# Kernel optimization log

Hardware: AMD Instinct MI355X
Metric: run time of the kernel (lower is better)

Reference implementation:

```python
import jax, jax.numpy as jnp
import numpy as np

LN_EPS = 1e-5

def setup_inputs() -> dict:
    key = jax.random.key(0)
    ks = jax.random.split(key, 7)
    B, S, D = 16, 2048, 512
    scale_g = 1.0 / np.sqrt(2 * D)
    scale_c = 1.0 / np.sqrt(2 * D)
    return {
        "points": jax.random.normal(ks[0], (B, S, D), dtype=jnp.float32),
        "W_gate": jax.random.uniform(ks[1], (2 * D, 2 * D), jnp.float32, -scale_g, scale_g),
        "b_gate": jax.random.uniform(ks[2], (2 * D,), jnp.float32, -scale_g, scale_g),
        "W_cand": jax.random.uniform(ks[3], (2 * D, D), jnp.float32, -scale_c, scale_c),
        "b_cand": jax.random.uniform(ks[4], (D,), jnp.float32, -scale_c, scale_c),
        "gamma": jnp.ones((D,), jnp.float32),
        "beta": jnp.zeros((D,), jnp.float32),
    }

def _layer_norm(x, gamma, beta):
    mu = jnp.mean(x, axis=-1, keepdims=True)
    var = jnp.mean(jnp.square(x - mu), axis=-1, keepdims=True)
    return (x - mu) * jax.lax.rsqrt(var + LN_EPS) * gamma + beta

def reference(points, W_gate, b_gate, W_cand, b_cand, gamma, beta):
    B, S, D = points.shape
    h0 = jnp.zeros((B, D), dtype=points.dtype)

    def step(h, p_t):  # p_t: [B, D]
        combined = jnp.concatenate([p_t, h], axis=1)          # [B, 2D]
        gates = combined @ W_gate + b_gate                    # [B, 2D]
        r = jax.nn.sigmoid(gates[:, :D])
        z = jax.nn.sigmoid(gates[:, D:])
        cand_in = jnp.concatenate([p_t, r * h], axis=1)       # [B, 2D]
        c = jnp.tanh(cand_in @ W_cand + b_cand)               # [B, D]
        h_new = (1.0 - z) * h + z * c
        return h_new, h_new

    _, states = jax.lax.scan(step, h0, jnp.swapaxes(points, 0, 1))  # [S, B, D]
    states = jnp.swapaxes(states, 0, 1)                             # [B, S, D]
    displacement = states - points
    deformed = points + displacement
    return _layer_norm(deformed, gamma, beta)
```

## Files before the change

kernel.cpp:

```cpp
#include <hip/hip_runtime.h>


typedef _Float16 half8 __attribute__((ext_vector_type(8)));
typedef _Float16 half4 __attribute__((ext_vector_type(4)));
typedef float floatx4 __attribute__((ext_vector_type(4)));
typedef int int4v __attribute__((ext_vector_type(4)));

#define NBLK 16
#define TPB 256
#define S_LEN 2048

#define SZ_WPK (96ull * 16 * 64 * 8 * 2)
#define OFF_WHPK 0ull
#define OFF_WXPK (OFF_WHPK + SZ_WPK)
#define OFF_HBUF (OFF_WXPK + SZ_WPK)
#define OFF_CNT (OFF_HBUF + 16384ull)
#define OFF_RH (OFF_CNT + 16384ull)
#define OFF_XGT (OFF_RH + 16384ull)

__device__ __forceinline__ float sigmoid_f(float x) {
  return 1.f / (1.f + __expf(-x));
}
__device__ __forceinline__ float tanh_f(float x) {
  x = fminf(15.f, fmaxf(-15.f, x));
  float e = __expf(2.f * x);
  return (e - 1.f) / (e + 1.f);
}

__device__ __forceinline__ void ld4_cg(const _Float16* p, int4v (&f)[4]) {
  asm volatile(
      "global_load_dwordx4 %0, %4, off sc0 sc1\n\t"
      "global_load_dwordx4 %1, %4, off offset:64 sc0 sc1\n\t"
      "global_load_dwordx4 %2, %4, off offset:128 sc0 sc1\n\t"
      "global_load_dwordx4 %3, %4, off offset:192 sc0 sc1\n\t"
      "s_waitcnt vmcnt(0)"
      : "=&v"(f[0]), "=&v"(f[1]), "=&v"(f[2]), "=&v"(f[3])
      : "v"(p)
      : "memory");
}
__device__ __forceinline__ void st_cg_u16(_Float16* p, _Float16 v) {
  unsigned u = (unsigned)__builtin_bit_cast(unsigned short, v);
  asm volatile("global_store_short %0, %1, off sc0 sc1" ::"v"(p), "v"(u)
               : "memory");
}
__device__ __forceinline__ void vwait() {
  asm volatile("s_waitcnt vmcnt(0)" ::: "memory");
}
__device__ __forceinline__ void st_flag(unsigned* p, unsigned v) {
  asm volatile("global_store_dword %0, %1, off sc0 sc1" ::"v"(p), "v"(v)
               : "memory");
}
__device__ __forceinline__ unsigned ld_flag(const unsigned* p) {
  unsigned v;
  asm volatile("global_load_dword %0, %1, off sc0 sc1\n\t"
               "s_waitcnt vmcnt(0)"
               : "=v"(v)
               : "v"(p)
               : "memory");
  return v;
}

__device__ __forceinline__ void gbar(unsigned* __restrict__ flags, int j,
                                     unsigned token, int wave, int lane) {
  __syncthreads();
  if (wave == 0) {
    if (lane == 0) st_flag(flags + j, token);
    const unsigned* fp = flags + (lane & 15);
    for (;;) {
      unsigned v = ld_flag(fp);
      if (__all((int)(v >= token))) break;
    }
  }
  __syncthreads();
}

__global__ void pack_kernel(const float* __restrict__ Wg,
                            const float* __restrict__ Wc,
                            _Float16* __restrict__ Whpk,
                            _Float16* __restrict__ Wxpk) {
  int unit = blockIdx.x * 4 + (threadIdx.x >> 6);
  int lane = threadIdx.x & 63;
  int set = (unit >= 1536) ? 1 : 0;
  int rem = unit - set * 1536;
  int tile = rem >> 4, kc = rem & 15;
  int kb = kc * 32 + ((lane >> 4) << 3);
  int n = lane & 15;
  int row0 = set ? 0 : 512;
  half8 w;
  if (tile < 64) {
    int col = tile * 16 + n;
#pragma unroll
    for (int jj = 0; jj < 8; ++jj)
      w[jj] = (_Float16)Wg[(size_t)(row0 + kb + jj) * 1024 + col];
  } else {
    int col = (tile - 64) * 16 + n;
#pragma unroll
    for (int jj = 0; jj < 8; ++jj)
      w[jj] = (_Float16)Wc[(size_t)(row0 + kb + jj) * 512 + col];
  }
  _Float16* dst = set ? Wxpk : Whpk;
  *(half8*)(dst + ((size_t)rem * 64 + lane) * 8) = w;
}

__global__ __launch_bounds__(TPB) void xgemm_kernel(
    const float* __restrict__ points, const float* __restrict__ b_gate,
    const float* __restrict__ b_cand, const _Float16* __restrict__ Wxpk,
    _Float16* __restrict__ xgt) {
  __shared__ _Float16 x_lds[16][520];
  const int tid = threadIdx.x;
  const int wave = tid >> 6, lane = tid & 63;
  const int ln15 = lane & 15, q = lane >> 4;
  const int t = blockIdx.x;
  const int m = tid & 15, ch = tid >> 4;

  const float* xp = points + ((size_t)m * S_LEN + t) * 512 + ch * 32;
#pragma unroll
  for (int u = 0; u < 4; ++u) {
    float4 f0 = ((const float4*)xp)[2 * u];
    float4 f1 = ((const float4*)xp)[2 * u + 1];
    half8 hv;
    hv[0] = (_Float16)f0.x; hv[1] = (_Float16)f0.y;
    hv[2] = (_Float16)f0.z; hv[3] = (_Float16)f0.w;
    hv[4] = (_Float16)f1.x; hv[5] = (_Float16)f1.y;
    hv[6] = (_Float16)f1.z; hv[7] = (_Float16)f1.w;
    *(half8*)&x_lds[m][ch * 32 + u * 8] = hv;
  }
  __syncthreads();

  for (int tile = wave; tile < 96; tile += 4) {
    const _Float16* W = Wxpk + (size_t)tile * 8192;
    floatx4 a0 = {0.f, 0.f, 0.f, 0.f}, a1 = {0.f, 0.f, 0.f, 0.f};
#pragma unroll
    for (int kc = 0; kc < 16; kc += 2) {
      a0 = __builtin_amdgcn_mfma_f32_16x16x32_f16(
          *(const half8*)&x_lds[ln15][kc * 32 + q * 8],
          *(const half8*)(W + ((size_t)kc * 64 + lane) * 8), a0, 0, 0, 0);
      a1 = __builtin_amdgcn_mfma_f32_16x16x32_f16(
          *(const half8*)&x_lds[ln15][(kc + 1) * 32 + q * 8],
          *(const half8*)(W + ((size_t)(kc + 1) * 64 + lane) * 8), a1, 0, 0, 0);
    }
    float bias = (tile < 64) ? b_gate[tile * 16 + ln15]
                             : b_cand[(tile - 64) * 16 + ln15];
    half4 o;
#pragma unroll
    for (int i = 0; i < 4; ++i) o[i] = (_Float16)(a0[i] + a1[i] + bias);
    *(half4*)(xgt + (((size_t)t * 96 + tile) * 16 + ln15) * 16 + q * 4) = o;
  }
}

__global__ __launch_bounds__(TPB, 1) void rec_kernel(
    const _Float16* __restrict__ Whpk, const _Float16* __restrict__ xgt,
    _Float16* __restrict__ h_buf, _Float16* __restrict__ rh_buf,
    unsigned* __restrict__ flags, float* __restrict__ out) {
  __shared__ int4v hsh[1024];
  __shared__ float z_lds[16][36];

  const int tid = threadIdx.x;
  const int wave = tid >> 6, lane = tid & 63;
  const int ln15 = lane & 15, q = lane >> 4;
  const int j = blockIdx.x;

  const int twA = (wave < 2) ? (2 * j + wave) : (32 + 2 * j + (wave - 2));
  const int twB = 64 + 2 * j + (wave & 1);
  const int colA = 32 * j + 16 * (wave & 1) + ln15;

  half8 wA[16], wB[16];
  {
    const _Float16* sA = Whpk + (size_t)twA * 8192 + lane * 8;
#pragma unroll
    for (int kc = 0; kc < 16; ++kc) wA[kc] = *(const half8*)(sA + kc * 512);
  }
  if (wave < 2) {
    const _Float16* sB = Whpk + (size_t)twB * 8192 + lane * 8;
#pragma unroll
    for (int kc = 0; kc < 16; ++kc) wB[kc] = *(const half8*)(sB + kc * 512);
  }

  const _Float16* h_stage = h_buf + ln15 * 512 + q * 8 + wave * 128;
  const _Float16* rh_stage = rh_buf + ln15 * 512 + q * 8 + wave * 128;
  _Float16* rh_st = rh_buf + (q * 4) * 512 + colA;
  _Float16* h_st = h_buf + (q * 4) * 512 + colA;

  const _Float16* xga_p = xgt + ((size_t)twA * 16 + ln15) * 16 + q * 4;
  const _Float16* xcb_p = xgt + ((size_t)twB * 16 + ln15) * 16 + q * 4;
  half4 xga = *(const half4*)xga_p;
  half4 xcb = {0, 0, 0, 0};
  if (wave < 2) xcb = *(const half4*)xcb_p;

  float hreg[4] = {0.f, 0.f, 0.f, 0.f};

  for (int t = 0; t < S_LEN; ++t) {
    const size_t pn = (size_t)((t + 1 < S_LEN) ? t + 1 : t) * 24576;

    {
      int4v f[4];
      ld4_cg(h_stage, f);
#pragma unroll
      for (int u = 0; u < 4; ++u) hsh[(4 * wave + u) * 64 + lane] = f[u];
    }
    __syncthreads();

    floatx4 a0 = {0.f, 0.f, 0.f, 0.f}, a1 = {0.f, 0.f, 0.f, 0.f};
#pragma unroll
    for (int kc = 0; kc < 16; kc += 2) {
      a0 = __builtin_amdgcn_mfma_f32_16x16x32_f16(
          __builtin_bit_cast(half8, hsh[kc * 64 + lane]), wA[kc], a0, 0, 0, 0);
      a1 = __builtin_amdgcn_mfma_f32_16x16x32_f16(
          __builtin_bit_cast(half8, hsh[(kc + 1) * 64 + lane]), wA[kc + 1], a1,
          0, 0, 0);
    }
    if (wave < 2) {
#pragma unroll
      for (int i = 0; i < 4; ++i) {
        float r = sigmoid_f(a0[i] + a1[i] + (float)xga[i]);
        st_cg_u16(rh_st + i * 512, (_Float16)(r * hreg[i]));
      }
      vwait();
    } else {
#pragma unroll
      for (int i = 0; i < 4; ++i)
        z_lds[q * 4 + i][16 * (wave - 2) + ln15] =
            sigmoid_f(a0[i] + a1[i] + (float)xga[i]);
    }
    gbar(flags, j, 2u * t + 1u, wave, lane);

    {
      int4v f[4];
      ld4_cg(rh_stage, f);
#pragma unroll
      for (int u = 0; u < 4; ++u) hsh[(4 * wave + u) * 64 + lane] = f[u];
    }
    __syncthreads();

    if (wave < 2) {
      floatx4 b0 = {0.f, 0.f, 0.f, 0.f}, b1 = {0.f, 0.f, 0.f, 0.f};
#pragma unroll
      for (int kc = 0; kc < 16; kc += 2) {
        b0 = __builtin_amdgcn_mfma_f32_16x16x32_f16(
            __builtin_bit_cast(half8, hsh[kc * 64 + lane]), wB[kc], b0, 0, 0,
            0);
        b1 = __builtin_amdgcn_mfma_f32_16x16x32_f16(
            __builtin_bit_cast(half8, hsh[(kc + 1) * 64 + lane]), wB[kc + 1],
            b1, 0, 0, 0);
      }
      float hn_s[4];
#pragma unroll
      for (int i = 0; i < 4; ++i) {
        float cv = tanh_f(b0[i] + b1[i] + (float)xcb[i]);
        float zz = z_lds[q * 4 + i][16 * wave + ln15];
        float hn = hreg[i] + zz * (cv - hreg[i]);
        _Float16 hh = (_Float16)hn;
        hreg[i] = (float)hh;
        st_cg_u16(h_st + i * 512, hh);
        hn_s[i] = hn;
      }
      vwait();
      xga = *(const half4*)(xga_p + pn);
      xcb = *(const half4*)(xcb_p + pn);
#pragma unroll
      for (int i = 0; i < 4; ++i)
        out[((size_t)(q * 4 + i) * S_LEN + t) * 512 + colA] = hn_s[i];
    } else {
      xga = *(const half4*)(xga_p + pn);
    }
    gbar(flags, j, 2u * t + 2u, wave, lane);
  }
}

__global__ void ln_kernel(float* __restrict__ out, const float* __restrict__ gamma,
                          const float* __restrict__ beta) {
  int gw = (blockIdx.x * blockDim.x + threadIdx.x) >> 6;
  int lane = threadIdx.x & 63;
  int nw = (gridDim.x * blockDim.x) >> 6;
  float4 ga = ((const float4*)(gamma + lane * 8))[0];
  float4 gb = ((const float4*)(gamma + lane * 8))[1];
  float4 ba = ((const float4*)(beta + lane * 8))[0];
  float4 bb = ((const float4*)(beta + lane * 8))[1];
  for (int r = gw; r < 16 * S_LEN; r += nw) {
    float* p = out + (size_t)r * 512 + lane * 8;
    float4 v0 = ((float4*)p)[0], v1 = ((float4*)p)[1];
    float s = v0.x + v0.y + v0.z + v0.w + v1.x + v1.y + v1.z + v1.w;
    float sq = v0.x * v0.x + v0.y * v0.y + v0.z * v0.z + v0.w * v0.w +
               v1.x * v1.x + v1.y * v1.y + v1.z * v1.z + v1.w * v1.w;
#pragma unroll
    for (int off = 32; off > 0; off >>= 1) {
      s += __shfl_xor(s, off);
      sq += __shfl_xor(sq, off);
    }
    float mean = s * (1.f / 512.f);
    float var = sq * (1.f / 512.f) - mean * mean;
    float rstd = rsqrtf(var + 1e-5f);
    v0.x = (v0.x - mean) * rstd * ga.x + ba.x;
    v0.y = (v0.y - mean) * rstd * ga.y + ba.y;
    v0.z = (v0.z - mean) * rstd * ga.z + ba.z;
    v0.w = (v0.w - mean) * rstd * ga.w + ba.w;
    v1.x = (v1.x - mean) * rstd * gb.x + bb.x;
    v1.y = (v1.y - mean) * rstd * gb.y + bb.y;
    v1.z = (v1.z - mean) * rstd * gb.z + bb.z;
    v1.w = (v1.w - mean) * rstd * gb.w + bb.w;
    ((float4*)p)[0] = v0;
    ((float4*)p)[1] = v1;
  }
}

extern "C" void kernel_launch(void* const* d_in, const int* in_sizes, int n_in,
                              void* d_out, int out_size, void* d_ws,
                              size_t ws_size, hipStream_t stream) {
  const float* points = (const float*)d_in[0];
  const float* W_gate = (const float*)d_in[1];
  const float* b_gate = (const float*)d_in[2];
  const float* W_cand = (const float*)d_in[3];
  const float* b_cand = (const float*)d_in[4];
  const float* gamma = (const float*)d_in[5];
  const float* beta = (const float*)d_in[6];
  char* ws = (char*)d_ws;
  _Float16* Whpk = (_Float16*)(ws + OFF_WHPK);
  _Float16* Wxpk = (_Float16*)(ws + OFF_WXPK);
  _Float16* h_buf = (_Float16*)(ws + OFF_HBUF);
  unsigned* flags = (unsigned*)(ws + OFF_CNT);
  _Float16* rh_buf = (_Float16*)(ws + OFF_RH);
  _Float16* xgt = (_Float16*)(ws + OFF_XGT);
  float* out = (float*)d_out;

  hipMemsetAsync(ws + OFF_HBUF, 0, 32768, stream);
  pack_kernel<<<768, 256, 0, stream>>>(W_gate, W_cand, Whpk, Wxpk);
  xgemm_kernel<<<S_LEN, TPB, 0, stream>>>(points, b_gate, b_cand, Wxpk, xgt);
  rec_kernel<<<NBLK, TPB, 0, stream>>>(Whpk, xgt, h_buf, rh_buf, flags, out);
  ln_kernel<<<512, 256, 0, stream>>>(out, gamma, beta);
}
```

Before: 11.04 ms.

## Replace global flag barriers with token-tagged data words for dataflow sync

Removes the two grid-wide flag barriers per timestep. Each fp16 value of h and r*h is now stored in a 32-bit word whose upper 16 bits hold the timestep token, so consumers poll the data itself until every token matches, and no separate barrier is needed. The z gate gets a small done-flag and a double-buffered LDS slot, and all waves load the full h vector directly into registers instead of staging it through LDS. The intent is to cut the per-step latency of the serial recurrence, at the cost of doubled exchange bytes, heavier polling loads and more register pressure.

```diff
diff --git a/kernel.cpp b/kernel.cpp
--- a/kernel.cpp
+++ b/kernel.cpp
@@ -14,9 +14,9 @@
 #define OFF_WHPK 0ull
 #define OFF_WXPK (OFF_WHPK + SZ_WPK)
 #define OFF_HBUF (OFF_WXPK + SZ_WPK)
-#define OFF_CNT (OFF_HBUF + 16384ull)
+#define OFF_CNT (OFF_HBUF + 32768ull)
 #define OFF_RH (OFF_CNT + 16384ull)
-#define OFF_XGT (OFF_RH + 16384ull)
+#define OFF_XGT (OFF_RH + 32768ull)
 
 __device__ __forceinline__ float sigmoid_f(float x) {
   return 1.f / (1.f + __expf(-x));
@@ -27,51 +27,99 @@
   return (e - 1.f) / (e + 1.f);
 }
 
-__device__ __forceinline__ void ld4_cg(const _Float16* p, int4v (&f)[4]) {
+__device__ __forceinline__ void ld16a(const unsigned* p, int4v (&d)[16]) {
   asm volatile(
-      "global_load_dwordx4 %0, %4, off sc0 sc1\n\t"
-      "global_load_dwordx4 %1, %4, off offset:64 sc0 sc1\n\t"
-      "global_load_dwordx4 %2, %4, off offset:128 sc0 sc1\n\t"
-      "global_load_dwordx4 %3, %4, off offset:192 sc0 sc1\n\t"
-      "s_waitcnt vmcnt(0)"
-      : "=&v"(f[0]), "=&v"(f[1]), "=&v"(f[2]), "=&v"(f[3])
+      "global_load_dwordx4 %0,  %16, off sc0 sc1\n\t"
+      "global_load_dwordx4 %1,  %16, off offset:16 sc0 sc1\n\t"
+      "global_load_dwordx4 %2,  %16, off offset:128 sc0 sc1\n\t"
+      "global_load_dwordx4 %3,  %16, off offset:144 sc0 sc1\n\t"
+      "global_load_dwordx4 %4,  %16, off offset:256 sc0 sc1\n\t"
+      "global_load_dwordx4 %5,  %16, off offset:272 sc0 sc1\n\t"
+      "global_load_dwordx4 %6,  %16, off offset:384 sc0 sc1\n\t"
+      "global_load_dwordx4 %7,  %16, off offset:400 sc0 sc1\n\t"
+      "global_load_dwordx4 %8,  %16, off offset:512 sc0 sc1\n\t"
+      "global_load_dwordx4 %9,  %16, off offset:528 sc0 sc1\n\t"
+      "global_load_dwordx4 %10, %16, off offset:640 sc0 sc1\n\t"
+      "global_load_dwordx4 %11, %16, off offset:656 sc0 sc1\n\t"
+      "global_load_dwordx4 %12, %16, off offset:768 sc0 sc1\n\t"
+      "global_load_dwordx4 %13, %16, off offset:784 sc0 sc1\n\t"
+      "global_load_dwordx4 %14, %16, off offset:896 sc0 sc1\n\t"
+      "global_load_dwordx4 %15, %16, off offset:912 sc0 sc1"
+      : "=&v"(d[0]), "=&v"(d[1]), "=&v"(d[2]), "=&v"(d[3]), "=&v"(d[4]),
+        "=&v"(d[5]), "=&v"(d[6]), "=&v"(d[7]), "=&v"(d[8]), "=&v"(d[9]),
+        "=&v"(d[10]), "=&v"(d[11]), "=&v"(d[12]), "=&v"(d[13]), "=&v"(d[14]),
+        "=&v"(d[15])
       : "v"(p)
       : "memory");
 }
-__device__ __forceinline__ void st_cg_u16(_Float16* p, _Float16 v) {
-  unsigned u = (unsigned)__builtin_bit_cast(unsigned short, v);
-  asm volatile("global_store_short %0, %1, off sc0 sc1" ::"v"(p), "v"(u)
-               : "memory");
-}
-__device__ __forceinline__ void vwait() {
-  asm volatile("s_waitcnt vmcnt(0)" ::: "memory");
-}
-__device__ __forceinline__ void st_flag(unsigned* p, unsigned v) {
+__device__ __forceinline__ void ld16b(const unsigned* p, int4v (&d)[16]) {
+  asm volatile(
+      "global_load_dwordx4 %0,  %16, off offset:1024 sc0 sc1\n\t"
+      "global_load_dwordx4 %1,  %16, off offset:1040 sc0 sc1\n\t"
+      "global_load_dwordx4 %2,  %16, off offset:1152 sc0 sc1\n\t"
+      "global_load_dwordx4 %3,  %16, off offset:1168 sc0 sc1\n\t"
+      "global_load_dwordx4 %4,  %16, off offset:1280 sc0 sc1\n\t"
+      "global_load_dwordx4 %5,  %16, off offset:1296 sc0 sc1\n\t"
+      "global_load_dwordx4 %6,  %16, off offset:1408 sc0 sc1\n\t"
+      "global_load_dwordx4 %7,  %16, off offset:1424 sc0 sc1\n\t"
+      "global_load_dwordx4 %8,  %16, off offset:1536 sc0 sc1\n\t"
+      "global_load_dwordx4 %9,  %16, off offset:1552 sc0 sc1\n\t"
+      "global_load_dwordx4 %10, %16, off offset:1664 sc0 sc1\n\t"
+      "global_load_dwordx4 %11, %16, off offset:1680 sc0 sc1\n\t"
+      "global_load_dwordx4 %12, %16, off offset:1792 sc0 sc1\n\t"
+      "global_load_dwordx4 %13, %16, off offset:1808 sc0 sc1\n\t"
+      "global_load_dwordx4 %14, %16, off offset:1920 sc0 sc1\n\t"
+      "global_load_dwordx4 %15, %16, off offset:1936 sc0 sc1\n\t"
+      "s_waitcnt vmcnt(0)"
+      : "=&v"(d[0]), "=&v"(d[1]), "=&v"(d[2]), "=&v"(d[3]), "=&v"(d[4]),
+        "=&v"(d[5]), "=&v"(d[6]), "=&v"(d[7]), "=&v"(d[8]), "=&v"(d[9]),
+        "=&v"(d[10]), "=&v"(d[11]), "=&v"(d[12]), "=&v"(d[13]), "=&v"(d[14]),
+        "=&v"(d[15])
+      : "v"(p)
+      : "memory");
+}
+__device__ __forceinline__ void ld16bz(const unsigned* p, const unsigned* zp,
+                                       int4v (&d)[16], unsigned& zd) {
+  asm volatile(
+      "global_load_dwordx4 %0,  %17, off offset:1024 sc0 sc1\n\t"
+      "global_load_dwordx4 %1,  %17, off offset:1040 sc0 sc1\n\t"
+      "global_load_dwordx4 %2,  %17, off offset:1152 sc0 sc1\n\t"
+      "global_load_dwordx4 %3,  %17, off offset:1168 sc0 sc1\n\t"
+      "global_load_dwordx4 %4,  %17, off offset:1280 sc0 sc1\n\t"
+      "global_load_dwordx4 %5,  %17, off offset:1296 sc0 sc1\n\t"
+      "global_load_dwordx4 %6,  %17, off offset:1408 sc0 sc1\n\t"
+      "global_load_dwordx4 %7,  %17, off offset:1424 sc0 sc1\n\t"
+      "global_load_dwordx4 %8,  %17, off offset:1536 sc0 sc1\n\t"
+      "global_load_dwordx4 %9,  %17, off offset:1552 sc0 sc1\n\t"
+      "global_load_dwordx4 %10, %17, off offset:1664 sc0 sc1\n\t"
+      "global_load_dwordx4 %11, %17, off offset:1680 sc0 sc1\n\t"
+      "global_load_dwordx4 %12, %17, off offset:1792 sc0 sc1\n\t"
+      "global_load_dwordx4 %13, %17, off offset:1808 sc0 sc1\n\t"
+      "global_load_dwordx4 %14, %17, off offset:1920 sc0 sc1\n\t"
+      "global_load_dwordx4 %15, %17, off offset:1936 sc0 sc1\n\t"
+      "global_load_dword   %16, %18, off sc0 sc1\n\t"
+      "s_waitcnt vmcnt(0)"
+      : "=&v"(d[0]), "=&v"(d[1]), "=&v"(d[2]), "=&v"(d[3]), "=&v"(d[4]),
+        "=&v"(d[5]), "=&v"(d[6]), "=&v"(d[7]), "=&v"(d[8]), "=&v"(d[9]),
+        "=&v"(d[10]), "=&v"(d[11]), "=&v"(d[12]), "=&v"(d[13]), "=&v"(d[14]),
+        "=&v"(d[15]), "=&v"(zd)
+      : "v"(p), "v"(zp)
+      : "memory");
+}
+__device__ __forceinline__ void st_dw(unsigned* p, unsigned v) {
   asm volatile("global_store_dword %0, %1, off sc0 sc1" ::"v"(p), "v"(v)
                : "memory");
 }
-__device__ __forceinline__ unsigned ld_flag(const unsigned* p) {
-  unsigned v;
-  asm volatile("global_load_dword %0, %1, off sc0 sc1\n\t"
-               "s_waitcnt vmcnt(0)"
-               : "=v"(v)
-               : "v"(p)
-               : "memory");
-  return v;
-}
-
-__device__ __forceinline__ void gbar(unsigned* __restrict__ flags, int j,
-                                     unsigned token, int wave, int lane) {
-  __syncthreads();
-  if (wave == 0) {
-    if (lane == 0) st_flag(flags + j, token);
-    const unsigned* fp = flags + (lane & 15);
-    for (;;) {
-      unsigned v = ld_flag(fp);
-      if (__all((int)(v >= token))) break;
-    }
-  }
-  __syncthreads();
+__device__ __forceinline__ unsigned pk2(unsigned p1, unsigned p0) {
+  return __builtin_amdgcn_perm(p1, p0, 0x05040100u);
+}
+__device__ __forceinline__ half8 unpk(int4v lo, int4v hi) {
+  int4v f;
+  f[0] = (int)pk2((unsigned)lo[1], (unsigned)lo[0]);
+  f[1] = (int)pk2((unsigned)lo[3], (unsigned)lo[2]);
+  f[2] = (int)pk2((unsigned)hi[1], (unsigned)hi[0]);
+  f[3] = (int)pk2((unsigned)hi[3], (unsigned)hi[2]);
+  return __builtin_bit_cast(half8, f);
 }
 
 __global__ void pack_kernel(const float* __restrict__ Wg,
@@ -150,10 +198,9 @@
 
 __global__ __launch_bounds__(TPB, 1) void rec_kernel(
     const _Float16* __restrict__ Whpk, const _Float16* __restrict__ xgt,
-    _Float16* __restrict__ h_buf, _Float16* __restrict__ rh_buf,
-    unsigned* __restrict__ flags, float* __restrict__ out) {
-  __shared__ int4v hsh[1024];
-  __shared__ float z_lds[16][36];
+    unsigned* __restrict__ h2, unsigned* __restrict__ rh2,
+    unsigned* __restrict__ zdone, float* __restrict__ out) {
+  __shared__ float z_lds[2][16][36];
 
   const int tid = threadIdx.x;
   const int wave = tid >> 6, lane = tid & 63;
@@ -176,10 +223,11 @@
     for (int kc = 0; kc < 16; ++kc) wB[kc] = *(const half8*)(sB + kc * 512);
   }
 
-  const _Float16* h_stage = h_buf + ln15 * 512 + q * 8 + wave * 128;
-  const _Float16* rh_stage = rh_buf + ln15 * 512 + q * 8 + wave * 128;
-  _Float16* rh_st = rh_buf + (q * 4) * 512 + colA;
-  _Float16* h_st = h_buf + (q * 4) * 512 + colA;
+  const unsigned* h2rd = h2 + ln15 * 512 + q * 8;
+  const unsigned* rh2rd = rh2 + ln15 * 512 + q * 8;
+  unsigned* rh2wr = rh2 + (q * 4) * 512 + colA;
+  unsigned* h2wr = h2 + (q * 4) * 512 + colA;
+  const unsigned* zdp = zdone + (lane & 31);
 
   const _Float16* xga_p = xgt + ((size_t)twA * 16 + ln15) * 16 + q * 4;
   const _Float16* xcb_p = xgt + ((size_t)twB * 16 + ln15) * 16 + q * 4;
@@ -191,79 +239,113 @@
 
   for (int t = 0; t < S_LEN; ++t) {
     const size_t pn = (size_t)((t + 1 < S_LEN) ? t + 1 : t) * 24576;
-
+    const unsigned tok1 = (unsigned)t + 1u;
+    const unsigned tokhi1 = tok1 << 16;
+
+    int4v dlo[16], dhi[16];
     {
-      int4v f[4];
-      ld4_cg(h_stage, f);
-#pragma unroll
-      for (int u = 0; u < 4; ++u) hsh[(4 * wave + u) * 64 + lane] = f[u];
-    }
-    __syncthreads();
-
+      const unsigned tokpat = ((unsigned)t) << 16;
+      for (;;) {
+        ld16a(h2rd, dlo);
+        ld16b(h2rd, dhi);
+        unsigned acc = 0;
+#pragma unroll
+        for (int u = 0; u < 16; ++u) {
+#pragma unroll
+          for (int c = 0; c < 4; ++c) {
+            acc |= (((unsigned)dlo[u][c]) ^ tokpat);
+            acc |= (((unsigned)dhi[u][c]) ^ tokpat);
+          }
+        }
+        if (__all((int)((acc >> 16) == 0u))) break;
+      }
+    }
     floatx4 a0 = {0.f, 0.f, 0.f, 0.f}, a1 = {0.f, 0.f, 0.f, 0.f};
 #pragma unroll
-    for (int kc = 0; kc < 16; kc += 2) {
+    for (int kc = 0; kc < 8; kc += 2) {
       a0 = __builtin_amdgcn_mfma_f32_16x16x32_f16(
-          __builtin_bit_cast(half8, hsh[kc * 64 + lane]), wA[kc], a0, 0, 0, 0);
+          unpk(dlo[2 * kc], dlo[2 * kc + 1]), wA[kc], a0, 0, 0, 0);
       a1 = __builtin_amdgcn_mfma_f32_16x16x32_f16(
-          __builtin_bit_cast(half8, hsh[(kc + 1) * 64 + lane]), wA[kc + 1], a1,
+          unpk(dlo[2 * kc + 2], dlo[2 * kc + 3]), wA[kc + 1], a1, 0, 0, 0);
+    }
+#pragma unroll
+    for (int kc = 8; kc < 16; kc += 2) {
+      a0 = __builtin_amdgcn_mfma_f32_16x16x32_f16(
+          unpk(dhi[2 * (kc - 8)], dhi[2 * (kc - 8) + 1]), wA[kc], a0, 0, 0, 0);
+      a1 = __builtin_amdgcn_mfma_f32_16x16x32_f16(
+          unpk(dhi[2 * (kc - 8) + 2], dhi[2 * (kc - 8) + 3]), wA[kc + 1], a1,
           0, 0, 0);
     }
+
     if (wave < 2) {
+      half4 xga_nx = *(const half4*)(xga_p + pn);
 #pragma unroll
       for (int i = 0; i < 4; ++i) {
         float r = sigmoid_f(a0[i] + a1[i] + (float)xga[i]);
-        st_cg_u16(rh_st + i * 512, (_Float16)(r * hreg[i]));
-      }
-      vwait();
+        unsigned hv = (unsigned)__builtin_bit_cast(
+            unsigned short, (_Float16)(r * hreg[i]));
+        st_dw(rh2wr + i * 512, tokhi1 | hv);
+      }
+      xga = xga_nx;
     } else {
+      if (lane == 0) st_dw(zdone + 2 * j + (wave - 2), tok1);
 #pragma unroll
       for (int i = 0; i < 4; ++i)
-        z_lds[q * 4 + i][16 * (wave - 2) + ln15] =
+        z_lds[t & 1][q * 4 + i][16 * (wave - 2) + ln15] =
             sigmoid_f(a0[i] + a1[i] + (float)xga[i]);
-    }
-    gbar(flags, j, 2u * t + 1u, wave, lane);
-
-    {
-      int4v f[4];
-      ld4_cg(rh_stage, f);
-#pragma unroll
-      for (int u = 0; u < 4; ++u) hsh[(4 * wave + u) * 64 + lane] = f[u];
+      xga = *(const half4*)(xga_p + pn);
     }
     __syncthreads();
 
     if (wave < 2) {
+      int4v elo[16], ehi[16];
+      unsigned zd;
+      for (;;) {
+        ld16a(rh2rd, elo);
+        ld16bz(rh2rd, zdp, ehi, zd);
+        unsigned acc = 0;
+#pragma unroll
+        for (int u = 0; u < 16; ++u) {
+#pragma unroll
+          for (int c = 0; c < 4; ++c) {
+            acc |= (((unsigned)elo[u][c]) ^ tokhi1);
+            acc |= (((unsigned)ehi[u][c]) ^ tokhi1);
+          }
+        }
+        unsigned bad = (acc >> 16) | (unsigned)(zd < tok1);
+        if (__all((int)(bad == 0u))) break;
+      }
       floatx4 b0 = {0.f, 0.f, 0.f, 0.f}, b1 = {0.f, 0.f, 0.f, 0.f};
 #pragma unroll
-      for (int kc = 0; kc < 16; kc += 2) {
+      for (int kc = 0; kc < 8; kc += 2) {
         b0 = __builtin_amdgcn_mfma_f32_16x16x32_f16(
-            __builtin_bit_cast(half8, hsh[kc * 64 + lane]), wB[kc], b0, 0, 0,
+            unpk(elo[2 * kc], elo[2 * kc + 1]), wB[kc], b0, 0, 0, 0);
+        b1 = __builtin_amdgcn_mfma_f32_16x16x32_f16(
+            unpk(elo[2 * kc + 2], elo[2 * kc + 3]), wB[kc + 1], b1, 0, 0, 0);
+      }
+#pragma unroll
+      for (int kc = 8; kc < 16; kc += 2) {
+        b0 = __builtin_amdgcn_mfma_f32_16x16x32_f16(
+            unpk(ehi[2 * (kc - 8)], ehi[2 * (kc - 8) + 1]), wB[kc], b0, 0, 0,
             0);
         b1 = __builtin_amdgcn_mfma_f32_16x16x32_f16(
-            __builtin_bit_cast(half8, hsh[(kc + 1) * 64 + lane]), wB[kc + 1],
-            b1, 0, 0, 0);
-      }
-      float hn_s[4];
+            unpk(ehi[2 * (kc - 8) + 2], ehi[2 * (kc - 8) + 3]), wB[kc + 1], b1,
+            0, 0, 0);
+      }
+      half4 xcb_nx = *(const half4*)(xcb_p + pn);
 #pragma unroll
       for (int i = 0; i < 4; ++i) {
         float cv = tanh_f(b0[i] + b1[i] + (float)xcb[i]);
-        float zz = z_lds[q * 4 + i][16 * wave + ln15];
+        float zz = z_lds[t & 1][q * 4 + i][16 * wave + ln15];
         float hn = hreg[i] + zz * (cv - hreg[i]);
         _Float16 hh = (_Float16)hn;
         hreg[i] = (float)hh;
-        st_cg_u16(h_st + i * 512, hh);
-        hn_s[i] = hn;
-      }
-      vwait();
-      xga = *(const half4*)(xga_p + pn);
-      xcb = *(const half4*)(xcb_p + pn);
-#pragma unroll
-      for (int i = 0; i < 4; ++i)
-        out[((size_t)(q * 4 + i) * S_LEN + t) * 512 + colA] = hn_s[i];
-    } else {
-      xga = *(const half4*)(xga_p + pn);
-    }
-    gbar(flags, j, 2u * t + 2u, wave, lane);
+        unsigned hb = (unsigned)__builtin_bit_cast(unsigned short, hh);
+        st_dw(h2wr + i * 512, tokhi1 | hb);
+        out[((size_t)(q * 4 + i) * S_LEN + t) * 512 + colA] = hn;
+      }
+      xcb = xcb_nx;
+    }
   }
 }
 
@@ -316,15 +398,15 @@
   char* ws = (char*)d_ws;
   _Float16* Whpk = (_Float16*)(ws + OFF_WHPK);
   _Float16* Wxpk = (_Float16*)(ws + OFF_WXPK);
-  _Float16* h_buf = (_Float16*)(ws + OFF_HBUF);
-  unsigned* flags = (unsigned*)(ws + OFF_CNT);
-  _Float16* rh_buf = (_Float16*)(ws + OFF_RH);
+  unsigned* h2 = (unsigned*)(ws + OFF_HBUF);
+  unsigned* zdone = (unsigned*)(ws + OFF_CNT);
+  unsigned* rh2 = (unsigned*)(ws + OFF_RH);
   _Float16* xgt = (_Float16*)(ws + OFF_XGT);
   float* out = (float*)d_out;
 
-  hipMemsetAsync(ws + OFF_HBUF, 0, 32768, stream);
+  hipMemsetAsync(ws + OFF_HBUF, 0, 81920, stream);
   pack_kernel<<<768, 256, 0, stream>>>(W_gate, W_cand, Whpk, Wxpk);
   xgemm_kernel<<<S_LEN, TPB, 0, stream>>>(points, b_gate, b_cand, Wxpk, xgt);
-  rec_kernel<<<NBLK, TPB, 0, stream>>>(Whpk, xgt, h_buf, rh_buf, flags, out);
+  rec_kernel<<<NBLK, TPB, 0, stream>>>(Whpk, xgt, h2, rh2, zdone, out);
   ln_kernel<<<512, 256, 0, stream>>>(out, gamma, beta);
 }
```

After: 33.66 ms. 205% more time.

## Replace flag-based grid barriers with token-tagged data polling in recurrence

Applied to the files above, without the earlier changes.

Removes the two per-step global flag barriers in the recurrent kernel. Each fp16 hidden-state value is now stored as a 32-bit word carrying the step token in its upper half, and consumers spin on the data itself until every word has the expected token. This fuses synchronization with data transfer, saving a store/wait/poll round trip per phase. It doubles the exchanged buffer size, uses a double-buffered LDS staging area, and moves the next-step xgt loads earlier to overlap with compute.

```diff
diff --git a/kernel.cpp b/kernel.cpp
--- a/kernel.cpp
+++ b/kernel.cpp
@@ -14,9 +14,8 @@
 #define OFF_WHPK 0ull
 #define OFF_WXPK (OFF_WHPK + SZ_WPK)
 #define OFF_HBUF (OFF_WXPK + SZ_WPK)
-#define OFF_CNT (OFF_HBUF + 16384ull)
-#define OFF_RH (OFF_CNT + 16384ull)
-#define OFF_XGT (OFF_RH + 16384ull)
+#define OFF_RH (OFF_HBUF + 32768ull)
+#define OFF_XGT (OFF_RH + 32768ull)
 
 __device__ __forceinline__ float sigmoid_f(float x) {
   return 1.f / (1.f + __expf(-x));
@@ -27,51 +26,52 @@
   return (e - 1.f) / (e + 1.f);
 }
 
-__device__ __forceinline__ void ld4_cg(const _Float16* p, int4v (&f)[4]) {
+__device__ __forceinline__ void ld8_cg(const unsigned* p, int4v (&d)[8]) {
   asm volatile(
-      "global_load_dwordx4 %0, %4, off sc0 sc1\n\t"
-      "global_load_dwordx4 %1, %4, off offset:64 sc0 sc1\n\t"
-      "global_load_dwordx4 %2, %4, off offset:128 sc0 sc1\n\t"
-      "global_load_dwordx4 %3, %4, off offset:192 sc0 sc1\n\t"
+      "global_load_dwordx4 %0, %8, off sc0 sc1\n\t"
+      "global_load_dwordx4 %1, %8, off offset:16 sc0 sc1\n\t"
+      "global_load_dwordx4 %2, %8, off offset:128 sc0 sc1\n\t"
+      "global_load_dwordx4 %3, %8, off offset:144 sc0 sc1\n\t"
+      "global_load_dwordx4 %4, %8, off offset:256 sc0 sc1\n\t"
+      "global_load_dwordx4 %5, %8, off offset:272 sc0 sc1\n\t"
+      "global_load_dwordx4 %6, %8, off offset:384 sc0 sc1\n\t"
+      "global_load_dwordx4 %7, %8, off offset:400 sc0 sc1\n\t"
       "s_waitcnt vmcnt(0)"
-      : "=&v"(f[0]), "=&v"(f[1]), "=&v"(f[2]), "=&v"(f[3])
+      : "=&v"(d[0]), "=&v"(d[1]), "=&v"(d[2]), "=&v"(d[3]), "=&v"(d[4]),
+        "=&v"(d[5]), "=&v"(d[6]), "=&v"(d[7])
       : "v"(p)
       : "memory");
 }
-__device__ __forceinline__ void st_cg_u16(_Float16* p, _Float16 v) {
-  unsigned u = (unsigned)__builtin_bit_cast(unsigned short, v);
-  asm volatile("global_store_short %0, %1, off sc0 sc1" ::"v"(p), "v"(u)
-               : "memory");
-}
-__device__ __forceinline__ void vwait() {
-  asm volatile("s_waitcnt vmcnt(0)" ::: "memory");
-}
-__device__ __forceinline__ void st_flag(unsigned* p, unsigned v) {
+__device__ __forceinline__ void st_dw(unsigned* p, unsigned v) {
   asm volatile("global_store_dword %0, %1, off sc0 sc1" ::"v"(p), "v"(v)
                : "memory");
 }
-__device__ __forceinline__ unsigned ld_flag(const unsigned* p) {
-  unsigned v;
-  asm volatile("global_load_dword %0, %1, off sc0 sc1\n\t"
-               "s_waitcnt vmcnt(0)"
-               : "=v"(v)
-               : "v"(p)
-               : "memory");
-  return v;
-}
-
-__device__ __forceinline__ void gbar(unsigned* __restrict__ flags, int j,
-                                     unsigned token, int wave, int lane) {
-  __syncthreads();
-  if (wave == 0) {
-    if (lane == 0) st_flag(flags + j, token);
-    const unsigned* fp = flags + (lane & 15);
-    for (;;) {
-      unsigned v = ld_flag(fp);
-      if (__all((int)(v >= token))) break;
-    }
-  }
-  __syncthreads();
+__device__ __forceinline__ unsigned pk2(unsigned p1, unsigned p0) {
+  return __builtin_amdgcn_perm(p1, p0, 0x05040100u);
+}
+
+__device__ __forceinline__ void stage_val(const unsigned* p, unsigned tokhi,
+                                          int4v* lds_dst) {
+  int4v d[8];
+  for (;;) {
+    ld8_cg(p, d);
+    unsigned acc = 0;
+#pragma unroll
+    for (int u = 0; u < 8; ++u)
+#pragma unroll
+      for (int c = 0; c < 4; ++c) acc |= ((unsigned)d[u][c]) ^ tokhi;
+    if (__all((int)((acc >> 16) == 0u))) break;
+    __builtin_amdgcn_s_sleep(2);
+  }
+#pragma unroll
+  for (int u = 0; u < 4; ++u) {
+    int4v f;
+    f[0] = (int)pk2((unsigned)d[2 * u][1], (unsigned)d[2 * u][0]);
+    f[1] = (int)pk2((unsigned)d[2 * u][3], (unsigned)d[2 * u][2]);
+    f[2] = (int)pk2((unsigned)d[2 * u + 1][1], (unsigned)d[2 * u + 1][0]);
+    f[3] = (int)pk2((unsigned)d[2 * u + 1][3], (unsigned)d[2 * u + 1][2]);
+    lds_dst[u * 64] = f;
+  }
 }
 
 __global__ void pack_kernel(const float* __restrict__ Wg,
@@ -150,9 +150,9 @@
 
 __global__ __launch_bounds__(TPB, 1) void rec_kernel(
     const _Float16* __restrict__ Whpk, const _Float16* __restrict__ xgt,
-    _Float16* __restrict__ h_buf, _Float16* __restrict__ rh_buf,
-    unsigned* __restrict__ flags, float* __restrict__ out) {
-  __shared__ int4v hsh[1024];
+    unsigned* __restrict__ h2, unsigned* __restrict__ rh2,
+    float* __restrict__ out) {
+  __shared__ int4v hsh[2][1024];
   __shared__ float z_lds[16][36];
 
   const int tid = threadIdx.x;
@@ -176,10 +176,12 @@
     for (int kc = 0; kc < 16; ++kc) wB[kc] = *(const half8*)(sB + kc * 512);
   }
 
-  const _Float16* h_stage = h_buf + ln15 * 512 + q * 8 + wave * 128;
-  const _Float16* rh_stage = rh_buf + ln15 * 512 + q * 8 + wave * 128;
-  _Float16* rh_st = rh_buf + (q * 4) * 512 + colA;
-  _Float16* h_st = h_buf + (q * 4) * 512 + colA;
+  const unsigned* h2rd = h2 + ln15 * 512 + q * 8 + wave * 128;
+  const unsigned* rh2rd = rh2 + ln15 * 512 + q * 8 + wave * 128;
+  unsigned* rh2wr = rh2 + (q * 4) * 512 + colA;
+  unsigned* h2wr = h2 + (q * 4) * 512 + colA;
+  int4v* ldsA = &hsh[0][(4 * wave) * 64 + lane];
+  int4v* ldsB = &hsh[1][(4 * wave) * 64 + lane];
 
   const _Float16* xga_p = xgt + ((size_t)twA * 16 + ln15) * 16 + q * 4;
   const _Float16* xcb_p = xgt + ((size_t)twB * 16 + ln15) * 16 + q * 4;
@@ -191,45 +193,40 @@
 
   for (int t = 0; t < S_LEN; ++t) {
     const size_t pn = (size_t)((t + 1 < S_LEN) ? t + 1 : t) * 24576;
-
-    {
-      int4v f[4];
-      ld4_cg(h_stage, f);
-#pragma unroll
-      for (int u = 0; u < 4; ++u) hsh[(4 * wave + u) * 64 + lane] = f[u];
-    }
+    const unsigned tok1 = (unsigned)t + 1u;
+    const unsigned tokhi1 = tok1 << 16;
+
+    stage_val(h2rd, ((unsigned)t) << 16, ldsA);
     __syncthreads();
 
     floatx4 a0 = {0.f, 0.f, 0.f, 0.f}, a1 = {0.f, 0.f, 0.f, 0.f};
 #pragma unroll
     for (int kc = 0; kc < 16; kc += 2) {
       a0 = __builtin_amdgcn_mfma_f32_16x16x32_f16(
-          __builtin_bit_cast(half8, hsh[kc * 64 + lane]), wA[kc], a0, 0, 0, 0);
+          *(const half8*)&hsh[0][kc * 64 + lane], wA[kc], a0, 0, 0, 0);
       a1 = __builtin_amdgcn_mfma_f32_16x16x32_f16(
-          __builtin_bit_cast(half8, hsh[(kc + 1) * 64 + lane]), wA[kc + 1], a1,
-          0, 0, 0);
+          *(const half8*)&hsh[0][(kc + 1) * 64 + lane], wA[kc + 1], a1, 0, 0,
+          0);
     }
     if (wave < 2) {
+      half4 xga_nx = *(const half4*)(xga_p + pn);
 #pragma unroll
       for (int i = 0; i < 4; ++i) {
         float r = sigmoid_f(a0[i] + a1[i] + (float)xga[i]);
-        st_cg_u16(rh_st + i * 512, (_Float16)(r * hreg[i]));
+        unsigned hv = (unsigned)__builtin_bit_cast(unsigned short,
+                                                   (_Float16)(r * hreg[i]));
+        st_dw(rh2wr + i * 512, tokhi1 | hv);
       }
-      vwait();
+      xga = xga_nx;
     } else {
 #pragma unroll
       for (int i = 0; i < 4; ++i)
         z_lds[q * 4 + i][16 * (wave - 2) + ln15] =
             sigmoid_f(a0[i] + a1[i] + (float)xga[i]);
-    }
-    gbar(flags, j, 2u * t + 1u, wave, lane);
-
-    {
-      int4v f[4];
-      ld4_cg(rh_stage, f);
-#pragma unroll
-      for (int u = 0; u < 4; ++u) hsh[(4 * wave + u) * 64 + lane] = f[u];
-    }
+      xga = *(const half4*)(xga_p + pn);
+    }
+
+    stage_val(rh2rd, tokhi1, ldsB);
     __syncthreads();
 
     if (wave < 2) {
@@ -237,13 +234,12 @@
 #pragma unroll
       for (int kc = 0; kc < 16; kc += 2) {
         b0 = __builtin_amdgcn_mfma_f32_16x16x32_f16(
-            __builtin_bit_cast(half8, hsh[kc * 64 + lane]), wB[kc], b0, 0, 0,
+            *(const half8*)&hsh[1][kc * 64 + lane], wB[kc], b0, 0, 0, 0);
+        b1 = __builtin_amdgcn_mfma_f32_16x16x32_f16(
+            *(const half8*)&hsh[1][(kc + 1) * 64 + lane], wB[kc + 1], b1, 0, 0,
             0);
-        b1 = __builtin_amdgcn_mfma_f32_16x16x32_f16(
-            __builtin_bit_cast(half8, hsh[(kc + 1) * 64 + lane]), wB[kc + 1],
-            b1, 0, 0, 0);
       }
-      float hn_s[4];
+      half4 xcb_nx = *(const half4*)(xcb_p + pn);
 #pragma unroll
       for (int i = 0; i < 4; ++i) {
         float cv = tanh_f(b0[i] + b1[i] + (float)xcb[i]);
@@ -251,19 +247,12 @@
         float hn = hreg[i] + zz * (cv - hreg[i]);
         _Float16 hh = (_Float16)hn;
         hreg[i] = (float)hh;
-        st_cg_u16(h_st + i * 512, hh);
-        hn_s[i] = hn;
+        unsigned hb = (unsigned)__builtin_bit_cast(unsigned short, hh);
+        st_dw(h2wr + i * 512, tokhi1 | hb);
+        out[((size_t)(q * 4 + i) * S_LEN + t) * 512 + colA] = hn;
       }
-      vwait();
-      xga = *(const half4*)(xga_p + pn);
-      xcb = *(const half4*)(xcb_p + pn);
-#pragma unroll
-      for (int i = 0; i < 4; ++i)
-        out[((size_t)(q * 4 + i) * S_LEN + t) * 512 + colA] = hn_s[i];
-    } else {
-      xga = *(const half4*)(xga_p + pn);
-    }
-    gbar(flags, j, 2u * t + 2u, wave, lane);
+      xcb = xcb_nx;
+    }
   }
 }
 
@@ -316,15 +305,14 @@
   char* ws = (char*)d_ws;
   _Float16* Whpk = (_Float16*)(ws + OFF_WHPK);
   _Float16* Wxpk = (_Float16*)(ws + OFF_WXPK);
-  _Float16* h_buf = (_Float16*)(ws + OFF_HBUF);
-  unsigned* flags = (unsigned*)(ws + OFF_CNT);
-  _Float16* rh_buf = (_Float16*)(ws + OFF_RH);
+  unsigned* h2 = (unsigned*)(ws + OFF_HBUF);
+  unsigned* rh2 = (unsigned*)(ws + OFF_RH);
   _Float16* xgt = (_Float16*)(ws + OFF_XGT);
   float* out = (float*)d_out;
 
-  hipMemsetAsync(ws + OFF_HBUF, 0, 32768, stream);
+  hipMemsetAsync(ws + OFF_HBUF, 0, 65536, stream);
   pack_kernel<<<768, 256, 0, stream>>>(W_gate, W_cand, Whpk, Wxpk);
   xgemm_kernel<<<S_LEN, TPB, 0, stream>>>(points, b_gate, b_cand, Wxpk, xgt);
-  rec_kernel<<<NBLK, TPB, 0, stream>>>(Whpk, xgt, h_buf, rh_buf, flags, out);
+  rec_kernel<<<NBLK, TPB, 0, stream>>>(Whpk, xgt, h2, rh2, out);
   ln_kernel<<<512, 256, 0, stream>>>(out, gamma, beta);
 }
```

After: 12.59 ms. +14.0%, slower.
